# Performance work log

Hardware: AMD Instinct MI355X
Metric: run time of the kernel (lower is better)

Reference implementation:

```python
import jax, jax.numpy as jnp
import numpy as np

B, N_P, N_S, D, H = 8, 512, 512, 512, 8
HD = D // H
SCALE = HD ** -0.5


def setup_inputs() -> dict:
    key = jax.random.key(0)
    ks = jax.random.split(key, 16)
    init = lambda k, shape, fan_in: jax.random.normal(k, shape, jnp.float32) * (1.0 / np.sqrt(fan_in))
    return {
        "piece_embeds": jax.random.normal(ks[0], (B, N_P, D), jnp.float32),
        "slot_embeds": jax.random.normal(ks[1], (B, N_S, D), jnp.float32),
        "mask": jax.random.randint(ks[2], (B, N_P, N_S), 0, 2, jnp.int32),
        "spatial_bias": jax.random.normal(ks[3], (B, N_P, N_S), jnp.float32),
        "Wq": init(ks[4], (D, D), D), "bq": jnp.zeros((D,), jnp.float32),
        "Wk": init(ks[5], (D, D), D), "bk": jnp.zeros((D,), jnp.float32),
        "Wv": init(ks[6], (D, D), D), "bv": jnp.zeros((D,), jnp.float32),
        "Wo": init(ks[7], (D, D), D), "bo": jnp.zeros((D,), jnp.float32),
        "Wc": init(ks[8], (2 * D,), 2 * D), "bc": jnp.zeros((), jnp.float32),
        "Wval": init(ks[9], (D,), D), "bval": jnp.zeros((), jnp.float32),
    }


def reference(piece_embeds, slot_embeds, mask, spatial_bias,
              Wq, bq, Wk, bk, Wv, bv, Wo, bo, Wc, bc, Wval, bval):
    Bv, Np, Dv = piece_embeds.shape
    Ns = slot_embeds.shape[1]
    Q = (piece_embeds @ Wq + bq).reshape(Bv, Np, H, HD)
    K = (slot_embeds @ Wk + bk).reshape(Bv, Ns, H, HD)
    V = (slot_embeds @ Wv + bv).reshape(Bv, Ns, H, HD)
    # per-head scores, scaled, then averaged over heads (non-standard)
    scores = jnp.einsum('bphd,bshd->bps', Q, K) * (SCALE / H)
    scores = scores + spatial_bias
    scores = jnp.where(mask == 0, jnp.float32(-1e9), scores)
    attn_probs = jax.nn.softmax(scores, axis=-1)  # dropout is identity at eval
    # the original expand*mul*sum over [B,Np,Ns,H,HD] == this contraction
    attn_output = jnp.einsum('bps,bshd->bphd', attn_probs, V).reshape(Bv, Np, Dv)
    output = attn_output @ Wo + bo
    value = (output.mean(axis=1) @ Wval + bval)[:, None]  # [B,1]
    # concat-linear over pairs == split-weight GEMMs with broadcast add
    Wc_p, Wc_s = Wc[:Dv], Wc[Dv:]
    compatibility = (piece_embeds @ Wc_p)[:, :, None] + (slot_embeds @ Wc_s)[:, None, :] + bc
    return scores, value, compatibility
```

## Files before the change

kernel.cpp:

```cpp
#include <hip/hip_runtime.h>
#include <math.h>

#define NP 512
#define NS 512
#define DD 512
#define INV64 0.015625f
#define NEGBIG -1000000000.0f
#define LOG2E 1.4426950408889634f

#define WS_MTBF   0
#define WS_TBF    131072
#define WS_PBF    1179648
#define WS_SBF    2228224
#define WS_WQBF   3276800
#define WS_WKBF   3407872
#define WS_WV     3538944
#define WS_U      3539456
#define WS_WQBK   3539968
#define WS_WKBQ   3540480
#define WS_VV     3540992
#define WS_A      3545088
#define WS_E      3549184
#define WS_CP     3553280
#define WS_CS     3557376
#define WS_Z      3561472
#define WS_W      3565568
#define WS_SC     3569664

#define OUT_SCORES 0
#define OUT_VALUE  2097152
#define OUT_COMP   2097160

typedef short bf16x8 __attribute__((ext_vector_type(8)));
typedef float f32x4 __attribute__((ext_vector_type(4)));

__device__ __forceinline__ short f2bf(float f) {
  unsigned u = __builtin_bit_cast(unsigned, f);
  u += 0x7fffu + ((u >> 16) & 1u);
  return (short)(u >> 16);
}

__device__ __forceinline__ void async_copy16(const void* g, void* l) {
  __builtin_amdgcn_global_load_lds(
      (const __attribute__((address_space(1))) unsigned int*)g,
      (__attribute__((address_space(3))) unsigned int*)l, 16, 0, 0);
}

__device__ __forceinline__ float dot8(float4 a0, float4 a1, float4 b0, float4 b1) {
  return a0.x * b0.x + a0.y * b0.y + a0.z * b0.z + a0.w * b0.w +
         a1.x * b1.x + a1.y * b1.y + a1.z * b1.z + a1.w * b1.w;
}

__device__ __forceinline__ float wave_red(float s) {
#pragma unroll
  for (int o = 32; o; o >>= 1) s += __shfl_xor(s, o);
  return s;
}

__device__ inline float wave_dot512(const float* __restrict__ x,
                                    const float* __restrict__ y, int lane) {
  float4 x0 = *(const float4*)&x[lane * 8];
  float4 x1 = *(const float4*)&x[lane * 8 + 4];
  float4 y0 = *(const float4*)&y[lane * 8];
  float4 y1 = *(const float4*)&y[lane * 8 + 4];
  return wave_red(dot8(x0, x1, y0, y1));
}

__global__ __launch_bounds__(256) void kA(
    const float* __restrict__ Wo, const float* __restrict__ Wval,
    const float* __restrict__ Wq, const float* __restrict__ bk,
    const float* __restrict__ Wk, const float* __restrict__ bq,
    const float* __restrict__ bo, const float* __restrict__ bval,
    float* __restrict__ ws, short* __restrict__ wqb, short* __restrict__ wkb) {
  int blk = blockIdx.x;
  if (blk < 385) {
    int wid = blk * 4 + (threadIdx.x >> 6);
    int lane = threadIdx.x & 63;
    if (wid >= 1538) return;
    const float *x, *y;
    float* dst;
    float extra = 0.f;
    int r = wid & 511;
    if (wid < 512)        { x = Wo + (size_t)r * DD; y = Wval; dst = ws + WS_WV + r; }
    else if (wid < 1024)  { x = Wq + (size_t)r * DD; y = bk;   dst = ws + WS_WQBK + r; }
    else if (wid < 1536)  { x = Wk + (size_t)r * DD; y = bq;   dst = ws + WS_WKBQ + r; }
    else if (wid == 1536) { x = bo; y = Wval; dst = ws + WS_SC + 1; extra = *bval; }
    else                  { x = bq; y = bk;   dst = ws + WS_SC + 2; }
    float s = wave_dot512(x, y, lane);
    if (lane == 0) *dst = s + extra;
  } else {
    int t = (blk - 385) * 256 + threadIdx.x;
    const float* src;
    short* dst;
    int off;
    if (t < 32768) { src = Wq; dst = wqb; off = t * 8; }
    else           { src = Wk; dst = wkb; off = (t - 32768) * 8; }
    float4 v0 = *(const float4*)&src[off];
    float4 v1 = *(const float4*)&src[off + 4];
    bf16x8 o;
    o[0] = f2bf(v0.x); o[1] = f2bf(v0.y); o[2] = f2bf(v0.z); o[3] = f2bf(v0.w);
    o[4] = f2bf(v1.x); o[5] = f2bf(v1.y); o[6] = f2bf(v1.z); o[7] = f2bf(v1.w);
    *(bf16x8*)&dst[off] = o;
  }
}

template <int MODE>
__global__ __launch_bounds__(256) void k64(
    const short* __restrict__ A, const short* __restrict__ B,
    short* __restrict__ Cb, const float* __restrict__ Wv,
    const float* __restrict__ bv, float* __restrict__ ws,
    const float* __restrict__ sbias, const int* __restrict__ maskp,
    const float* __restrict__ bc, float* __restrict__ out) {
  __shared__ alignas(16) short As[2][64 * 64];
  __shared__ alignas(16) short Bs[2][64 * 64];
  const int wave = threadIdx.x >> 6, lane = threadIdx.x & 63;
  const int id = blockIdx.x;

  if (MODE == 0 && id >= 64) {
    int wid = (id - 64) * 4 + wave;
    if (wid > 512) return;
    if (wid < 512) {
      float s = wave_dot512(Wv + (size_t)wid * DD, ws + WS_WV, lane);
      if (lane == 0) ws[WS_U + wid] = s;
    } else {
      float s = wave_dot512(bv, ws + WS_WV, lane);
      if (lane == 0) ws[WS_SC + 0] = s;
    }
    return;
  }

  const int wr = wave >> 1, wc = wave & 1;
  const int li = lane & 15, g = lane >> 4;
  int b = 0, m0, n0;
  if (MODE == 0)      { m0 = (id & 7) * 64; n0 = (id >> 3) * 64; }
  else if (MODE == 1) { m0 = (id & 63) * 64; n0 = (id >> 6) * 64; }
  else                { b = id & 7; m0 = ((id >> 6) & 7) * 64; n0 = ((id >> 3) & 7) * 64; }
  const short* Ab = A + (size_t)b * NP * DD;
  const short* Bb = B + (size_t)b * NS * DD;
  f32x4 acc[2][2] = {};

  auto stage = [&](int bufi, int k0) {
#pragma unroll
    for (int h = 0; h < 2; ++h) {
      int s = h * 256 + threadIdx.x;
      int row = s >> 3;
      int gsrc = (s & 7) ^ (row & 7);
      async_copy16(Ab + (size_t)(m0 + row) * DD + k0 + gsrc * 8, &As[bufi][s * 8]);
      async_copy16(Bb + (size_t)(n0 + row) * DD + k0 + gsrc * 8, &Bs[bufi][s * 8]);
    }
  };

  stage(0, 0);
  __syncthreads();
  int buf = 0;
  for (int k0 = 0; k0 < DD; k0 += 64) {
    if (k0 + 64 < DD) stage(buf ^ 1, k0 + 64);
    bf16x8 af[2][2], bfv[2][2];
#pragma unroll
    for (int kk = 0; kk < 2; ++kk) {
#pragma unroll
      for (int am = 0; am < 2; ++am) {
        int row = wr * 32 + am * 16 + li;
        af[am][kk] = *(const bf16x8*)&As[buf][(row * 8 + ((kk * 4 + g) ^ (row & 7))) * 8];
      }
#pragma unroll
      for (int bn = 0; bn < 2; ++bn) {
        int row = wc * 32 + bn * 16 + li;
        bfv[bn][kk] = *(const bf16x8*)&Bs[buf][(row * 8 + ((kk * 4 + g) ^ (row & 7))) * 8];
      }
    }
#pragma unroll
    for (int kk = 0; kk < 2; ++kk)
#pragma unroll
      for (int am = 0; am < 2; ++am)
#pragma unroll
        for (int bn = 0; bn < 2; ++bn)
          acc[am][bn] = __builtin_amdgcn_mfma_f32_16x16x32_bf16(
              af[am][kk], bfv[bn][kk], acc[am][bn], 0, 0, 0);
    __syncthreads();
    buf ^= 1;
  }

  if (MODE != 2) {
#pragma unroll
    for (int am = 0; am < 2; ++am)
#pragma unroll
      for (int i = 0; i < 4; ++i) {
        int grow = m0 + wr * 32 + am * 16 + g * 4 + i;
#pragma unroll
        for (int bn = 0; bn < 2; ++bn) {
          int gcol = n0 + wc * 32 + bn * 16 + li;
          Cb[(size_t)grow * DD + gcol] = f2bf(acc[am][bn][i]);
        }
      }
  } else {
    const float sbb = ws[WS_SC + 2];
    const float bcv = *bc;
    float ev[2], vvl[2], csl[2];
#pragma unroll
    for (int bn = 0; bn < 2; ++bn) {
      int scol = n0 + wc * 32 + bn * 16 + li;
      ev[bn] = ws[WS_E + b * NS + scol];
      vvl[bn] = ws[WS_VV + b * NS + scol];
      csl[bn] = ws[WS_CS + b * NS + scol];
    }
#pragma unroll
    for (int am = 0; am < 2; ++am)
#pragma unroll
      for (int i = 0; i < 4; ++i) {
        int p = m0 + wr * 32 + am * 16 + g * 4 + i;
        float av = ws[WS_A + b * NP + p] + sbb;
        float cpv = ws[WS_CP + b * NP + p] + bcv;
        float zp = 0.f, wp = 0.f;
#pragma unroll
        for (int bn = 0; bn < 2; ++bn) {
          int scol = n0 + wc * 32 + bn * 16 + li;
          size_t idx = ((size_t)b * NP + p) * NS + scol;
          float v = fmaf(acc[am][bn][i] + av + ev[bn], INV64, sbias[idx]);
          v = (maskp[idx] == 0) ? NEGBIG : v;
          out[OUT_SCORES + idx] = v;
          float ee = exp2f(v * LOG2E);
          zp += ee;
          wp += ee * vvl[bn];
          out[OUT_COMP + idx] = cpv + csl[bn];
        }
#pragma unroll
        for (int o = 1; o < 16; o <<= 1) {
          zp += __shfl_xor(zp, o);
          wp += __shfl_xor(wp, o);
        }
        if (li == 0) {
          atomicAdd(&ws[WS_Z + b * NP + p], zp);
          atomicAdd(&ws[WS_W + b * NP + p], wp);
        }
      }
  }
}

__global__ __launch_bounds__(256) void kC(
    const float* __restrict__ piece, const float* __restrict__ slot,
    const float* __restrict__ Wc, float* __restrict__ ws,
    short* __restrict__ pbf, short* __restrict__ sbf) {
  int lane = threadIdx.x & 63;
  if (blockIdx.x < 1024) {
    int wid = blockIdx.x * 4 + (threadIdx.x >> 6);
    const float* row = piece + (size_t)wid * DD;
    float4 x0 = *(const float4*)&row[lane * 8];
    float4 x1 = *(const float4*)&row[lane * 8 + 4];
    bf16x8 o;
    o[0] = f2bf(x0.x); o[1] = f2bf(x0.y); o[2] = f2bf(x0.z); o[3] = f2bf(x0.w);
    o[4] = f2bf(x1.x); o[5] = f2bf(x1.y); o[6] = f2bf(x1.z); o[7] = f2bf(x1.w);
    *(bf16x8*)&pbf[(size_t)wid * DD + lane * 8] = o;
    const float* y = ws + WS_WQBK;
    float4 y0 = *(const float4*)&y[lane * 8];
    float4 y1 = *(const float4*)&y[lane * 8 + 4];
    float4 c0 = *(const float4*)&Wc[lane * 8];
    float4 c1 = *(const float4*)&Wc[lane * 8 + 4];
    float da = wave_red(dot8(x0, x1, y0, y1));
    float dc = wave_red(dot8(x0, x1, c0, c1));
    if (lane == 0) { ws[WS_A + wid] = da; ws[WS_CP + wid] = dc; }
  } else if (blockIdx.x < 2048) {
    int wid = (blockIdx.x - 1024) * 4 + (threadIdx.x >> 6);
    const float* row = slot + (size_t)wid * DD;
    float4 x0 = *(const float4*)&row[lane * 8];
    float4 x1 = *(const float4*)&row[lane * 8 + 4];
    bf16x8 o;
    o[0] = f2bf(x0.x); o[1] = f2bf(x0.y); o[2] = f2bf(x0.z); o[3] = f2bf(x0.w);
    o[4] = f2bf(x1.x); o[5] = f2bf(x1.y); o[6] = f2bf(x1.z); o[7] = f2bf(x1.w);
    *(bf16x8*)&sbf[(size_t)wid * DD + lane * 8] = o;
    const float* y = ws + WS_WKBQ;
    float4 y0 = *(const float4*)&y[lane * 8];
    float4 y1 = *(const float4*)&y[lane * 8 + 4];
    const float* u = ws + WS_U;
    float4 u0 = *(const float4*)&u[lane * 8];
    float4 u1 = *(const float4*)&u[lane * 8 + 4];
    const float* c = Wc + DD;
    float4 c0 = *(const float4*)&c[lane * 8];
    float4 c1 = *(const float4*)&c[lane * 8 + 4];
    float de = wave_red(dot8(x0, x1, y0, y1));
    float dv = wave_red(dot8(x0, x1, u0, u1));
    float dc = wave_red(dot8(x0, x1, c0, c1));
    if (lane == 0) {
      ws[WS_E + wid] = de;
      ws[WS_VV + wid] = dv + ws[WS_SC + 0];
      ws[WS_CS + wid] = dc;
    }
  } else {
    float4 zz = make_float4(0.f, 0.f, 0.f, 0.f);
#pragma unroll
    for (int k = 0; k < 8; ++k)
      *(float4*)&ws[WS_Z + (threadIdx.x * 8 + k) * 4] = zz;
  }
}

__global__ __launch_bounds__(512) void kG(const float* __restrict__ ws,
                                          float* __restrict__ out) {
  int vb = threadIdx.x >> 6, l = threadIdx.x & 63;
  const float* zp = ws + WS_Z + vb * NP;
  const float* wp = ws + WS_W + vb * NP;
  float s = 0.f;
#pragma unroll
  for (int j = 0; j < 8; ++j) {
    int p = l + j * 64;
    s += wp[p] / zp[p];
  }
#pragma unroll
  for (int o = 32; o; o >>= 1) s += __shfl_xor(s, o);
  if (l == 0) out[OUT_VALUE + vb] = s * (1.0f / NP) + ws[WS_SC + 1];
}

extern "C" void kernel_launch(void* const* d_in, const int* in_sizes, int n_in,
                              void* d_out, int out_size, void* d_ws,
                              size_t ws_size, hipStream_t stream) {
  const float* piece = (const float*)d_in[0];
  const float* slot = (const float*)d_in[1];
  const int* mask = (const int*)d_in[2];
  const float* sbias = (const float*)d_in[3];
  const float* Wq = (const float*)d_in[4];
  const float* bq = (const float*)d_in[5];
  const float* Wk = (const float*)d_in[6];
  const float* bk = (const float*)d_in[7];
  const float* Wv = (const float*)d_in[8];
  const float* bv = (const float*)d_in[9];
  const float* Wo = (const float*)d_in[10];
  const float* bo = (const float*)d_in[11];
  const float* Wc = (const float*)d_in[12];
  const float* bc = (const float*)d_in[13];
  const float* Wval = (const float*)d_in[14];
  const float* bval = (const float*)d_in[15];
  float* out = (float*)d_out;
  float* ws = (float*)d_ws;

  short* mtb = (short*)(ws + WS_MTBF);
  short* tbf = (short*)(ws + WS_TBF);
  short* pbf = (short*)(ws + WS_PBF);
  short* sbf = (short*)(ws + WS_SBF);
  short* wqb = (short*)(ws + WS_WQBF);
  short* wkb = (short*)(ws + WS_WKBF);

  hipLaunchKernelGGL(kA, dim3(641), dim3(256), 0, stream,
                     Wo, Wval, Wq, bk, Wk, bq, bo, bval, ws, wqb, wkb);
  hipLaunchKernelGGL((k64<0>), dim3(193), dim3(256), 0, stream,
                     wkb, wqb, mtb, Wv, bv, ws,
                     (const float*)nullptr, (const int*)nullptr,
                     (const float*)nullptr, (float*)nullptr);
  hipLaunchKernelGGL(kC, dim3(2049), dim3(256), 0, stream, piece, slot, Wc, ws,
                     pbf, sbf);
  hipLaunchKernelGGL((k64<1>), dim3(512), dim3(256), 0, stream,
                     pbf, mtb, tbf, (const float*)nullptr, (const float*)nullptr,
                     ws, (const float*)nullptr, (const int*)nullptr,
                     (const float*)nullptr, (float*)nullptr);
  hipLaunchKernelGGL((k64<2>), dim3(512), dim3(256), 0, stream,
                     tbf, sbf, (short*)nullptr, (const float*)nullptr,
                     (const float*)nullptr, ws, sbias, mask, bc, out);
  hipLaunchKernelGGL(kG, dim3(1), dim3(512), 0, stream, ws, out);
}
```

Baseline: 48.86 us.

## Remap block indices for XCD locality and prefetch bias/mask during last K step

The MODE 1 GEMM and the kC conversion kernel now remap blockIdx so that consecutive blocks with the same id mod 8 (likely one XCD under round-robin dispatch) handle contiguous rows. The aim is better L2 locality per XCD. In MODE 2, the spatial_bias and mask loads are issued during the final K iteration, before the last MFMAs, so their latency overlaps compute instead of sitting in the epilogue. The trailing __syncthreads is also skipped after the last iteration. This costs extra registers to hold the prefetched values, which may lower occupancy.

```diff
diff --git a/kernel.cpp b/kernel.cpp
--- a/kernel.cpp
+++ b/kernel.cpp
@@ -132,12 +132,20 @@
   const int wr = wave >> 1, wc = wave & 1;
   const int li = lane & 15, g = lane >> 4;
   int b = 0, m0, n0;
-  if (MODE == 0)      { m0 = (id & 7) * 64; n0 = (id >> 3) * 64; }
-  else if (MODE == 1) { m0 = (id & 63) * 64; n0 = (id >> 6) * 64; }
-  else                { b = id & 7; m0 = ((id >> 6) & 7) * 64; n0 = ((id >> 3) & 7) * 64; }
+  if (MODE == 0) {
+    m0 = (id & 7) * 64; n0 = (id >> 3) * 64;
+  } else if (MODE == 1) {
+    int x = id & 7, r = id >> 3;
+    m0 = (x * 8 + (r >> 3)) * 64;
+    n0 = (r & 7) * 64;
+  } else {
+    b = id & 7; m0 = ((id >> 6) & 7) * 64; n0 = ((id >> 3) & 7) * 64;
+  }
   const short* Ab = A + (size_t)b * NP * DD;
   const short* Bb = B + (size_t)b * NS * DD;
   f32x4 acc[2][2] = {};
+  float sbr[2][4][2];
+  int mkr[2][4][2];
 
   auto stage = [&](int bufi, int k0) {
 #pragma unroll
@@ -154,7 +162,23 @@
   __syncthreads();
   int buf = 0;
   for (int k0 = 0; k0 < DD; k0 += 64) {
-    if (k0 + 64 < DD) stage(buf ^ 1, k0 + 64);
+    if (k0 + 64 < DD) {
+      stage(buf ^ 1, k0 + 64);
+    } else if (MODE == 2) {
+#pragma unroll
+      for (int am = 0; am < 2; ++am)
+#pragma unroll
+        for (int i = 0; i < 4; ++i) {
+          int p = m0 + wr * 32 + am * 16 + g * 4 + i;
+#pragma unroll
+          for (int bn = 0; bn < 2; ++bn) {
+            int scol = n0 + wc * 32 + bn * 16 + li;
+            size_t idx = ((size_t)b * NP + p) * NS + scol;
+            sbr[am][i][bn] = sbias[idx];
+            mkr[am][i][bn] = maskp[idx];
+          }
+        }
+    }
     bf16x8 af[2][2], bfv[2][2];
 #pragma unroll
     for (int kk = 0; kk < 2; ++kk) {
@@ -177,8 +201,10 @@
         for (int bn = 0; bn < 2; ++bn)
           acc[am][bn] = __builtin_amdgcn_mfma_f32_16x16x32_bf16(
               af[am][kk], bfv[bn][kk], acc[am][bn], 0, 0, 0);
-    __syncthreads();
-    buf ^= 1;
+    if (k0 + 64 < DD) {
+      __syncthreads();
+      buf ^= 1;
+    }
   }
 
   if (MODE != 2) {
@@ -216,8 +242,8 @@
         for (int bn = 0; bn < 2; ++bn) {
           int scol = n0 + wc * 32 + bn * 16 + li;
           size_t idx = ((size_t)b * NP + p) * NS + scol;
-          float v = fmaf(acc[am][bn][i] + av + ev[bn], INV64, sbias[idx]);
-          v = (maskp[idx] == 0) ? NEGBIG : v;
+          float v = fmaf(acc[am][bn][i] + av + ev[bn], INV64, sbr[am][i][bn]);
+          v = (mkr[am][i][bn] == 0) ? NEGBIG : v;
           out[OUT_SCORES + idx] = v;
           float ee = exp2f(v * LOG2E);
           zp += ee;
@@ -243,7 +269,10 @@
     short* __restrict__ pbf, short* __restrict__ sbf) {
   int lane = threadIdx.x & 63;
   if (blockIdx.x < 1024) {
-    int wid = blockIdx.x * 4 + (threadIdx.x >> 6);
+    int x = blockIdx.x & 7, r = blockIdx.x >> 3;
+    int q = x * 8 + (r >> 4);
+    int j = q * 16 + (r & 15);
+    int wid = j * 4 + (threadIdx.x >> 6);
     const float* row = piece + (size_t)wid * DD;
     float4 x0 = *(const float4*)&row[lane * 8];
     float4 x1 = *(const float4*)&row[lane * 8 + 4];
@@ -260,7 +289,10 @@
     float dc = wave_red(dot8(x0, x1, c0, c1));
     if (lane == 0) { ws[WS_A + wid] = da; ws[WS_CP + wid] = dc; }
   } else if (blockIdx.x < 2048) {
-    int wid = (blockIdx.x - 1024) * 4 + (threadIdx.x >> 6);
+    int t2 = (int)blockIdx.x - 1024;
+    int bb = t2 & 7, tt = t2 >> 3;
+    int j2 = bb * 128 + tt;
+    int wid = j2 * 4 + (threadIdx.x >> 6);
     const float* row = slot + (size_t)wid * DD;
     float4 x0 = *(const float4*)&row[lane * 8];
     float4 x1 = *(const float4*)&row[lane * 8 + 4];
```

Result: slower. 51.95 us (+6.3%).
